# Performance work log

Hardware: AMD Instinct MI355X
Metric: run time of the kernel (lower is better)

The kernel has to match this reference:

```python
import jax, jax.numpy as jnp
import numpy as np


def setup_inputs() -> dict:
    key = jax.random.key(0)
    k1, k2 = jax.random.split(key)
    pc1 = jax.random.normal(k1, (8, 2048, 3), dtype=jnp.float32)
    pc2 = jax.random.normal(k2, (8, 2048, 3), dtype=jnp.float32)
    return {"pc1": pc1, "pc2": pc2}


def reference(pc1, pc2):
    # Flatten to point lists, matching pc.reshape(-1, 3)
    p1 = pc1.reshape(-1, 3)  # [N1, 3]
    p2 = pc2.reshape(-1, 3)  # [N2, 3]
    # Squared pairwise distances via ||a||^2 + ||b||^2 - 2 a.b
    sq1 = jnp.sum(p1 * p1, axis=-1)  # [N1]
    sq2 = jnp.sum(p2 * p2, axis=-1)  # [N2]
    d2 = sq1[:, None] + sq2[None, :] - 2.0 * jnp.einsum('nd,md->nm', p1, p2)  # [N1, N2]
    d2 = jnp.maximum(d2, 0.0)
    d = jnp.sqrt(d2)  # Euclidean, matching cKDTree.query distances
    # dist1 = NN distance from each pc2 point into pc1 (tree1.query(pc2))
    dist1 = jnp.min(d, axis=0)  # [N2]
    # dist2 = NN distance from each pc1 point into pc2 (tree2.query(pc1))
    dist2 = jnp.min(d, axis=1)  # [N1]
    return jnp.mean(dist1) + jnp.mean(dist2)
```

## Files before the change

kernel.cpp:

```cpp
#include <hip/hip_runtime.h>
#include <math.h>

#define N_PTS 16384
#define TPB   256
#define IP    4
#define IBLK  (N_PTS / (TPB * IP))
#define JT    512
#define JS    (N_PTS / JT)
#define REDB  64

__global__ __launch_bounds__(TPB) void chamfer_pack(
    const float* __restrict__ p1, const float* __restrict__ p2,
    float4* __restrict__ P, unsigned int* __restrict__ dmin,
    float* __restrict__ outp) {
  int id = blockIdx.x * TPB + threadIdx.x;
  const float* src = (id < N_PTS) ? p1 : p2;
  int k = (id < N_PTS) ? id : (id - N_PTS);
  float x = src[3 * k + 0], y = src[3 * k + 1], z = src[3 * k + 2];
  P[id] = make_float4(x, y, z, 0.5f * (x * x + y * y + z * z));
  dmin[id] = 0x7F800000u;
  if (id == 0) outp[0] = 0.f;
}

__global__ __launch_bounds__(TPB) void chamfer_min(
    const float4* __restrict__ P, unsigned int* __restrict__ dmin) {
  __shared__ float4 tile[JT];
  const int dir = blockIdx.z;
  const float4* __restrict__ Q = P + (size_t)dir * N_PTS;
  const float4* __restrict__ T = P + (size_t)(1 - dir) * N_PTS;
  unsigned int* __restrict__ out = dmin + (size_t)dir * N_PTS;

  const int jbase = blockIdx.x * JT;
  for (int t = threadIdx.x; t < JT; t += TPB)
    tile[t] = T[jbase + t];
  __syncthreads();

  const int i0 = blockIdx.y * (TPB * IP) + threadIdx.x * IP;
  float nx[IP], ny[IP], nz[IP], cw[IP], vmin[IP];
#pragma unroll
  for (int k = 0; k < IP; ++k) {
    float4 p = Q[i0 + k];
    nx[k] = -p.x; ny[k] = -p.y; nz[k] = -p.z; cw[k] = p.w;
    vmin[k] = INFINITY;
  }

#pragma unroll 8
  for (int j = 0; j < JT; j += 2) {
    float4 qa = tile[j];
    float4 qb = tile[j + 1];
#pragma unroll
    for (int k = 0; k < IP; ++k) {
      float va = fmaf(nx[k], qa.x, qa.w);
      va = fmaf(ny[k], qa.y, va);
      va = fmaf(nz[k], qa.z, va);
      float vb = fmaf(nx[k], qb.x, qb.w);
      vb = fmaf(ny[k], qb.y, vb);
      vb = fmaf(nz[k], qb.z, vb);
      asm("v_min3_f32 %0, %1, %2, %3"
          : "=v"(vmin[k]) : "v"(va), "v"(vb), "v"(vmin[k]));
    }
  }

#pragma unroll
  for (int k = 0; k < IP; ++k) {
    float d2 = fmaxf(0.f, 2.f * (cw[k] + vmin[k]));
    atomicMin(&out[i0 + k], __float_as_uint(d2));
  }
}

__global__ __launch_bounds__(TPB) void chamfer_reduce(
    const unsigned int* __restrict__ dmin, float* __restrict__ outp) {
  float s = 0.f;
  for (int i = blockIdx.x * TPB + threadIdx.x; i < 2 * N_PTS; i += REDB * TPB)
    s += sqrtf(__uint_as_float(dmin[i]));
#pragma unroll
  for (int off = 32; off > 0; off >>= 1)
    s += __shfl_down(s, off, 64);
  __shared__ float partial[TPB / 64];
  if ((threadIdx.x & 63) == 0) partial[threadIdx.x >> 6] = s;
  __syncthreads();
  if (threadIdx.x == 0) {
    float t = 0.f;
    for (int w = 0; w < TPB / 64; ++w) t += partial[w];
    atomicAdd(outp, t * (1.0f / (float)N_PTS));
  }
}

extern "C" void kernel_launch(void* const* d_in, const int* in_sizes, int n_in,
                              void* d_out, int out_size, void* d_ws, size_t ws_size,
                              hipStream_t stream) {
  const float* pc1 = (const float*)d_in[0];
  const float* pc2 = (const float*)d_in[1];
  float4* P = (float4*)d_ws;
  unsigned int* dmin = (unsigned int*)((char*)d_ws + (size_t)2 * N_PTS * sizeof(float4));
  float* outp = (float*)d_out;

  chamfer_pack<<<(2 * N_PTS) / TPB, TPB, 0, stream>>>(pc1, pc2, P, dmin, outp);
  chamfer_min<<<dim3(JS, IBLK, 2), TPB, 0, stream>>>(P, dmin);
  chamfer_reduce<<<REDB, TPB, 0, stream>>>(dmin, outp);
}
```

Measured before the change: 99.52 us.

## Compute both nearest-neighbor directions in a single pass over the distance matrix

Instead of launching two passes (one per direction) over the full N×N distance grid, each tile now updates both the row minima (in registers) and the column minima (via a per-tile shared-memory atomicMin, flushed to global at the end). This halves the pairwise arithmetic. Point packing moves into the min kernel, which removes the separate pack pass and its workspace. Tile sizes change to 8 rows per thread and 128 columns per tile, with a rotated access order to spread the LDS atomics. The cost is per-iteration LDS atomics, extra min3 work, and more register pressure.

```diff
diff --git a/kernel.cpp b/kernel.cpp
--- a/kernel.cpp
+++ b/kernel.cpp
@@ -3,68 +3,84 @@
 
 #define N_PTS 16384
 #define TPB   256
-#define IP    4
-#define IBLK  (N_PTS / (TPB * IP))
-#define JT    512
+#define IP    8
+#define ROWS_B (TPB * IP)
+#define IBLK  (N_PTS / ROWS_B)
+#define JT    128
 #define JS    (N_PTS / JT)
+#define NCH   (JT / 2)
 #define REDB  64
 
-__global__ __launch_bounds__(TPB) void chamfer_pack(
-    const float* __restrict__ p1, const float* __restrict__ p2,
-    float4* __restrict__ P, unsigned int* __restrict__ dmin,
-    float* __restrict__ outp) {
+__global__ __launch_bounds__(TPB) void chamfer_init(
+    unsigned int* __restrict__ dmin, float* __restrict__ outp) {
   int id = blockIdx.x * TPB + threadIdx.x;
-  const float* src = (id < N_PTS) ? p1 : p2;
-  int k = (id < N_PTS) ? id : (id - N_PTS);
-  float x = src[3 * k + 0], y = src[3 * k + 1], z = src[3 * k + 2];
-  P[id] = make_float4(x, y, z, 0.5f * (x * x + y * y + z * z));
   dmin[id] = 0x7F800000u;
   if (id == 0) outp[0] = 0.f;
 }
 
-__global__ __launch_bounds__(TPB) void chamfer_min(
-    const float4* __restrict__ P, unsigned int* __restrict__ dmin) {
+__global__ __launch_bounds__(TPB, 4) void chamfer_min(
+    const float* __restrict__ p1, const float* __restrict__ p2,
+    unsigned int* __restrict__ dmin) {
   __shared__ float4 tile[JT];
-  const int dir = blockIdx.z;
-  const float4* __restrict__ Q = P + (size_t)dir * N_PTS;
-  const float4* __restrict__ T = P + (size_t)(1 - dir) * N_PTS;
-  unsigned int* __restrict__ out = dmin + (size_t)dir * N_PTS;
+  __shared__ unsigned int cmin[JT];
 
   const int jbase = blockIdx.x * JT;
-  for (int t = threadIdx.x; t < JT; t += TPB)
-    tile[t] = T[jbase + t];
+  for (int t = threadIdx.x; t < JT; t += TPB) {
+    float x = p2[3 * (jbase + t) + 0];
+    float y = p2[3 * (jbase + t) + 1];
+    float z = p2[3 * (jbase + t) + 2];
+    tile[t] = make_float4(x, y, z, 0.5f * (x * x + y * y + z * z));
+    cmin[t] = 0x7F800000u;
+  }
+
+  const int ibase = blockIdx.y * ROWS_B;
+  float nx[IP], ny[IP], nz[IP], h[IP], rmin[IP];
+#pragma unroll
+  for (int m = 0; m < IP; ++m) {
+    int r = ibase + m * TPB + threadIdx.x;
+    float x = p1[3 * r + 0], y = p1[3 * r + 1], z = p1[3 * r + 2];
+    nx[m] = -x; ny[m] = -y; nz[m] = -z;
+    h[m] = 0.5f * (x * x + y * y + z * z);
+    rmin[m] = INFINITY;
+  }
   __syncthreads();
 
-  const int i0 = blockIdx.y * (TPB * IP) + threadIdx.x * IP;
-  float nx[IP], ny[IP], nz[IP], cw[IP], vmin[IP];
+  const int base = (threadIdx.x & 63) + ((threadIdx.x >> 6) << 4);
+#pragma unroll 2
+  for (int s = 0; s < NCH; ++s) {
+    const int pos = (base + s) & (NCH - 1);
+    float4 qa = tile[pos];
+    float4 qb = tile[pos + NCH];
+    float cpa = INFINITY, cpb = INFINITY;
 #pragma unroll
-  for (int k = 0; k < IP; ++k) {
-    float4 p = Q[i0 + k];
-    nx[k] = -p.x; ny[k] = -p.y; nz[k] = -p.z; cw[k] = p.w;
-    vmin[k] = INFINITY;
-  }
-
-#pragma unroll 8
-  for (int j = 0; j < JT; j += 2) {
-    float4 qa = tile[j];
-    float4 qb = tile[j + 1];
-#pragma unroll
-    for (int k = 0; k < IP; ++k) {
-      float va = fmaf(nx[k], qa.x, qa.w);
-      va = fmaf(ny[k], qa.y, va);
-      va = fmaf(nz[k], qa.z, va);
-      float vb = fmaf(nx[k], qb.x, qb.w);
-      vb = fmaf(ny[k], qb.y, vb);
-      vb = fmaf(nz[k], qb.z, vb);
-      asm("v_min3_f32 %0, %1, %2, %3"
-          : "=v"(vmin[k]) : "v"(va), "v"(vb), "v"(vmin[k]));
+    for (int m = 0; m < IP; m += 2) {
+      float ta = h[m] + qa.w;
+      ta = fmaf(nx[m], qa.x, ta); ta = fmaf(ny[m], qa.y, ta); ta = fmaf(nz[m], qa.z, ta);
+      float tb = h[m] + qb.w;
+      tb = fmaf(nx[m], qb.x, tb); tb = fmaf(ny[m], qb.y, tb); tb = fmaf(nz[m], qb.z, tb);
+      float ua = h[m + 1] + qa.w;
+      ua = fmaf(nx[m + 1], qa.x, ua); ua = fmaf(ny[m + 1], qa.y, ua); ua = fmaf(nz[m + 1], qa.z, ua);
+      float ub = h[m + 1] + qb.w;
+      ub = fmaf(nx[m + 1], qb.x, ub); ub = fmaf(ny[m + 1], qb.y, ub); ub = fmaf(nz[m + 1], qb.z, ub);
+      asm("v_min3_f32 %0, %1, %2, %3" : "=v"(rmin[m])     : "v"(ta), "v"(tb), "v"(rmin[m]));
+      asm("v_min3_f32 %0, %1, %2, %3" : "=v"(rmin[m + 1]) : "v"(ua), "v"(ub), "v"(rmin[m + 1]));
+      asm("v_min3_f32 %0, %1, %2, %3" : "=v"(cpa)         : "v"(ta), "v"(ua), "v"(cpa));
+      asm("v_min3_f32 %0, %1, %2, %3" : "=v"(cpb)         : "v"(tb), "v"(ub), "v"(cpb));
     }
+    atomicMin(&cmin[pos],       __float_as_uint(fmaxf(cpa, 0.f)));
+    atomicMin(&cmin[pos + NCH], __float_as_uint(fmaxf(cpb, 0.f)));
   }
 
 #pragma unroll
-  for (int k = 0; k < IP; ++k) {
-    float d2 = fmaxf(0.f, 2.f * (cw[k] + vmin[k]));
-    atomicMin(&out[i0 + k], __float_as_uint(d2));
+  for (int m = 0; m < IP; ++m) {
+    float d2 = fmaxf(0.f, 2.f * rmin[m]);
+    atomicMin(&dmin[ibase + m * TPB + threadIdx.x], __float_as_uint(d2));
+  }
+
+  __syncthreads();
+  for (int t = threadIdx.x; t < JT; t += TPB) {
+    float v = __uint_as_float(cmin[t]);
+    atomicMin(&dmin[N_PTS + jbase + t], __float_as_uint(2.f * v));
   }
 }
 
@@ -91,11 +107,9 @@
                               hipStream_t stream) {
   const float* pc1 = (const float*)d_in[0];
   const float* pc2 = (const float*)d_in[1];
-  float4* P = (float4*)d_ws;
-  unsigned int* dmin = (unsigned int*)((char*)d_ws + (size_t)2 * N_PTS * sizeof(float4));
-  float* outp = (float*)d_out;
+  unsigned int* dmin = (unsigned int*)d_ws;
 
-  chamfer_pack<<<(2 * N_PTS) / TPB, TPB, 0, stream>>>(pc1, pc2, P, dmin, outp);
-  chamfer_min<<<dim3(JS, IBLK, 2), TPB, 0, stream>>>(P, dmin);
-  chamfer_reduce<<<REDB, TPB, 0, stream>>>(dmin, outp);
+  chamfer_init<<<(2 * N_PTS) / TPB, TPB, 0, stream>>>(dmin, (float*)d_out);
+  chamfer_min<<<dim3(JS, IBLK), TPB, 0, stream>>>(pc1, pc2, dmin);
+  chamfer_reduce<<<REDB, TPB, 0, stream>>>(dmin, (float*)d_out);
 }
```

Result: faster. 91.08 us (-8.5%).
